# Optimization experiments

Hardware: AMD Instinct MI355X
Metric: run time of the kernel (lower is better)

Reference implementation:

```python
import jax, jax.numpy as jnp
import numpy as np

B, L, D = 8, 2048, 64

def setup_inputs() -> dict:
    key = jax.random.key(0)
    k1, k2 = jax.random.split(key)
    query = jax.random.normal(k1, (B, L, D), dtype=jnp.float32)
    key_t = jax.random.normal(k2, (B, L, D), dtype=jnp.float32)
    return {"query": query, "key": key_t}

def reference(query, key):
    d = query.shape[-1]
    # scores: [B, Lq, Lk] = Q K^T / sqrt(d)
    scores = jnp.einsum('bqd,bkd->bqk', query, key) / jnp.sqrt(jnp.asarray(d, query.dtype))
    weights = jax.nn.softmax(scores, axis=-1)  # dropout p=0.0 -> identity
    # output uses `key` as values, matching the original module
    return jnp.einsum('bqk,bkd->bqd', weights, key)
```

## Files before the change

kernel.cpp:

```cpp
#include <hip/hip_runtime.h>
#include <hip/hip_bf16.h>


#define LL 2048
#define DD 64
#define BQ 128
#define BK 64
#define KPAD 72
#define NSEG 4
#define NQB (LL / BQ)

typedef __attribute__((ext_vector_type(8))) short bf16x8;
typedef __attribute__((ext_vector_type(4))) float f32x4;
typedef __attribute__((ext_vector_type(4))) unsigned short u16x4;

static __device__ __forceinline__ unsigned short f2bf(float f) {
  unsigned u = __builtin_bit_cast(unsigned, f);
  u += 0x7fffu + ((u >> 16) & 1u);
  return (unsigned short)(u >> 16);
}
static __device__ __forceinline__ float bf2f(unsigned short h) {
  unsigned u = (unsigned)h << 16;
  return __builtin_bit_cast(float, u);
}

__global__ __launch_bounds__(256, 3) void attn_kernel(
    const float* __restrict__ Q, const float* __restrict__ K,
    float* __restrict__ O, u16x4* __restrict__ Opart,
    float* __restrict__ Lp, int seglen, int nseg) {
  __shared__ __attribute__((aligned(16))) unsigned short sKt[2][BK][KPAD];
  __shared__ __attribute__((aligned(16))) unsigned short sKtT[2][DD * KPAD];
  __shared__ __attribute__((aligned(16))) unsigned short sP[4][16][KPAD];

  const int tid  = threadIdx.x;
  const int wave = tid >> 6;
  const int lane = tid & 63;
  const int quad = lane >> 4;
  const int l16  = lane & 15;

  const int batch = blockIdx.y;
  const int seg   = blockIdx.z;
  const int q0w   = blockIdx.x * BQ + wave * 32;
  const int ngroups = gridDim.y * NQB;
  const int gq    = batch * NQB + blockIdx.x;

  const float qs = 0.125f * 1.44269504f;
  bf16x8 bq[2][2];
#pragma unroll
  for (int qt = 0; qt < 2; ++qt) {
    const float* qrow = Q + (size_t)(batch * LL + q0w + qt * 16 + l16) * DD;
#pragma unroll
    for (int ks = 0; ks < 2; ++ks) {
      const float* p = qrow + ks * 32 + quad * 8;
      float4 f0 = *(const float4*)(p);
      float4 f1 = *(const float4*)(p + 4);
      bf16x8 a;
      a[0] = (short)f2bf(f0.x * qs); a[1] = (short)f2bf(f0.y * qs);
      a[2] = (short)f2bf(f0.z * qs); a[3] = (short)f2bf(f0.w * qs);
      a[4] = (short)f2bf(f1.x * qs); a[5] = (short)f2bf(f1.y * qs);
      a[6] = (short)f2bf(f1.z * qs); a[7] = (short)f2bf(f1.w * qs);
      bq[qt][ks] = a;
    }
  }

  f32x4 oacc[2][4];
  float l_part[2];
#pragma unroll
  for (int qt = 0; qt < 2; ++qt) {
#pragma unroll
    for (int n = 0; n < 4; ++n) oacc[qt][n] = (f32x4){0.f, 0.f, 0.f, 0.f};
    l_part[qt] = 0.f;
  }

  const int niter = seglen / BK;
  const float* kbase = K + (size_t)(batch * LL + seg * seglen) * DD;
  const int kv_o  = tid >> 3;
  const int oc_o  = tid & 7;
  const int kv_o2 = kv_o + 32;

  float4 pf[2][2];
#pragma unroll
  for (int i = 0; i < 2; ++i) {
    int p = tid + i * 256;
    const float4* src = (const float4*)(kbase + (size_t)(p >> 3) * DD + (p & 7) * 8);
    pf[i][0] = src[0];
    pf[i][1] = src[1];
  }
#pragma unroll
  for (int i = 0; i < 2; ++i) {
    int kv = i ? kv_o2 : kv_o, oc = oc_o;
    unsigned short h[8];
    h[0] = f2bf(pf[i][0].x); h[1] = f2bf(pf[i][0].y);
    h[2] = f2bf(pf[i][0].z); h[3] = f2bf(pf[i][0].w);
    h[4] = f2bf(pf[i][1].x); h[5] = f2bf(pf[i][1].y);
    h[6] = f2bf(pf[i][1].z); h[7] = f2bf(pf[i][1].w);
    *(bf16x8*)&sKt[0][kv][oc * 8] = *(const bf16x8*)h;
    int swz = ((kv >> 3) ^ oc) & 7;
    unsigned short* dst = &sKtT[0][(oc * 8) * KPAD + swz * 8 + (kv & 7)];
#pragma unroll
    for (int j = 0; j < 8; ++j) dst[j * KPAD] = h[j];
  }
  __syncthreads();

  for (int t = 0; t < niter; ++t) {
    const int cur = t & 1;
    const int nxt = cur ^ 1;

    if (t + 1 < niter) {
      const float* kt = kbase + (size_t)(t + 1) * BK * DD;
#pragma unroll
      for (int i = 0; i < 2; ++i) {
        int p = tid + i * 256;
        const float4* src = (const float4*)(kt + (size_t)(p >> 3) * DD + (p & 7) * 8);
        pf[i][0] = src[0];
        pf[i][1] = src[1];
      }
    }

    bf16x8 pa[2][2];
#pragma unroll
    for (int qt = 0; qt < 2; ++qt) {
      f32x4 s[4];
#pragma unroll
      for (int mt = 0; mt < 4; ++mt) {
        bf16x8 k0 = *(const bf16x8*)&sKt[cur][mt * 16 + l16][quad * 8];
        bf16x8 k1 = *(const bf16x8*)&sKt[cur][mt * 16 + l16][32 + quad * 8];
        f32x4 z = (f32x4){0.f, 0.f, 0.f, 0.f};
        s[mt] = __builtin_amdgcn_mfma_f32_16x16x32_bf16(k0, bq[qt][0], z, 0, 0, 0);
        s[mt] = __builtin_amdgcn_mfma_f32_16x16x32_bf16(k1, bq[qt][1], s[mt], 0, 0, 0);
      }
#pragma unroll
      for (int mt = 0; mt < 4; ++mt) {
        u16x4 h;
#pragma unroll
        for (int r = 0; r < 4; ++r) {
          float p = __builtin_amdgcn_exp2f(s[mt][r]);
          l_part[qt] += p;
          h[r] = f2bf(p);
        }
        *(u16x4*)&sP[wave][l16][mt * 16 + quad * 4] = h;
      }
      pa[qt][0] = *(const bf16x8*)&sP[wave][l16][quad * 8];
      pa[qt][1] = *(const bf16x8*)&sP[wave][l16][32 + quad * 8];
    }

    if (t + 1 < niter) {
#pragma unroll
      for (int i = 0; i < 2; ++i) {
        int kv = i ? kv_o2 : kv_o, oc = oc_o;
        unsigned short h[8];
        h[0] = f2bf(pf[i][0].x); h[1] = f2bf(pf[i][0].y);
        h[2] = f2bf(pf[i][0].z); h[3] = f2bf(pf[i][0].w);
        h[4] = f2bf(pf[i][1].x); h[5] = f2bf(pf[i][1].y);
        h[6] = f2bf(pf[i][1].z); h[7] = f2bf(pf[i][1].w);
        *(bf16x8*)&sKt[nxt][kv][oc * 8] = *(const bf16x8*)h;
        int swz = ((kv >> 3) ^ oc) & 7;
        unsigned short* dst = &sKtT[nxt][(oc * 8) * KPAD + swz * 8 + (kv & 7)];
#pragma unroll
        for (int j = 0; j < 8; ++j) dst[j * KPAD] = h[j];
      }
    }

#pragma unroll
    for (int ks = 0; ks < 2; ++ks)
#pragma unroll
      for (int nt = 0; nt < 4; ++nt) {
        int d = nt * 16 + l16;
        bf16x8 b = *(const bf16x8*)
            &sKtT[cur][d * KPAD + (((ks * 4 + quad) ^ (d >> 3)) & 7) * 8];
        oacc[0][nt] = __builtin_amdgcn_mfma_f32_16x16x32_bf16(pa[0][ks], b, oacc[0][nt], 0, 0, 0);
        oacc[1][nt] = __builtin_amdgcn_mfma_f32_16x16x32_bf16(pa[1][ks], b, oacc[1][nt], 0, 0, 0);
      }

    __syncthreads();
  }

#pragma unroll
  for (int qt = 0; qt < 2; ++qt) {
    l_part[qt] += __shfl_xor(l_part[qt], 16);
    l_part[qt] += __shfl_xor(l_part[qt], 32);
  }

  if (nseg == 1) {
#pragma unroll
    for (int qt = 0; qt < 2; ++qt)
#pragma unroll
      for (int r = 0; r < 4; ++r) {
        float lr = __shfl(l_part[qt], (lane & 48) | (quad * 4 + r), 64);
        float invl = 1.0f / lr;
        float* orow = O + (size_t)(batch * LL + q0w + qt * 16 + quad * 4 + r) * DD;
#pragma unroll
        for (int nt = 0; nt < 4; ++nt)
          orow[nt * 16 + l16] = oacc[qt][nt][r] * invl;
      }
    return;
  }

  const size_t slotbase = ((size_t)seg * ngroups + gq) * 32 + wave * 8;
#pragma unroll
  for (int qt = 0; qt < 2; ++qt) {
#pragma unroll
    for (int nt = 0; nt < 4; ++nt) {
      u16x4 h;
      h[0] = f2bf(oacc[qt][nt][0]); h[1] = f2bf(oacc[qt][nt][1]);
      h[2] = f2bf(oacc[qt][nt][2]); h[3] = f2bf(oacc[qt][nt][3]);
      Opart[(slotbase + qt * 4 + nt) * 64 + lane] = h;
    }
    if (quad == 0)
      Lp[(((size_t)seg * ngroups + gq) * 8 + wave * 2 + qt) * 16 + l16] = l_part[qt];
  }
}

__global__ __launch_bounds__(256) void combine_kernel(
    const u16x4* __restrict__ Opart, const float* __restrict__ Lp,
    float* __restrict__ O, int nseg, int ngroups) {
  const int tid  = threadIdx.x;
  const int g    = blockIdx.x;
  const int slot = blockIdx.y * 4 + (tid >> 6);
  const int lane = tid & 63;
  const int quad = lane >> 4;
  const int l16  = lane & 15;
  const int wv = slot >> 3, qt = (slot >> 2) & 1, nt = slot & 3;

  f32x4 acc = (f32x4){0.f, 0.f, 0.f, 0.f};
  float den = 0.f;
  for (int s = 0; s < nseg; ++s) {
    u16x4 h = Opart[((size_t)(s * ngroups + g) * 32 + slot) * 64 + lane];
    acc[0] += bf2f(h[0]); acc[1] += bf2f(h[1]);
    acc[2] += bf2f(h[2]); acc[3] += bf2f(h[3]);
    den += Lp[((size_t)(s * ngroups + g) * 8 + wv * 2 + qt) * 16 + l16];
  }
  const int batch = g / NQB, qbx = g % NQB;
  const int rowbase = batch * LL + qbx * BQ + wv * 32 + qt * 16;
#pragma unroll
  for (int r = 0; r < 4; ++r) {
    float dr = __shfl(den, (lane & 48) | (quad * 4 + r), 64);
    O[(size_t)(rowbase + quad * 4 + r) * DD + nt * 16 + l16] = acc[r] / dr;
  }
}

extern "C" void kernel_launch(void* const* d_in, const int* in_sizes, int n_in,
                              void* d_out, int out_size, void* d_ws, size_t ws_size,
                              hipStream_t stream) {
  const float* Q = (const float*)d_in[0];
  const float* K = (const float*)d_in[1];
  float* O = (float*)d_out;
  int B = in_sizes[0] / (LL * DD);
  int ngroups = B * NQB;

  size_t opart_bytes = (size_t)NSEG * ngroups * 32 * 64 * sizeof(u16x4);
  size_t lp_bytes    = (size_t)NSEG * ngroups * 8 * 16 * sizeof(float);
  if (ws_size >= opart_bytes + lp_bytes) {
    u16x4* Opart = (u16x4*)d_ws;
    float* Lpp = (float*)((char*)d_ws + opart_bytes);
    dim3 grid(NQB, B, NSEG);
    attn_kernel<<<grid, 256, 0, stream>>>(Q, K, O, Opart, Lpp, LL / NSEG, NSEG);
    combine_kernel<<<dim3(ngroups, 8), 256, 0, stream>>>(Opart, Lpp, O, NSEG, ngroups);
  } else {
    dim3 grid(NQB, B, 1);
    attn_kernel<<<grid, 256, 0, stream>>>(Q, K, O, nullptr, nullptr, LL, 1);
  }
}
```

Baseline: 81.36 us.

## Switch attention to 32x32x16 MFMA with in-register P via permlane swap

Replaces the 16x16x32 MFMA tiles with 32x32x16 MFMA so each wave handles 32 query rows as one tile. The softmax probabilities are packed with v_cvt_pk_bf16_f32 and rearranged into the A-operand layout with v_permlane32_swap, which removes the shared-memory round trip through sP. Float-to-bf16 conversions also use the packed hardware convert, and the partial-output and denominator layouts plus the combine kernel are updated to match. This relies on gfx950-specific instructions and needs more accumulator registers per wave, which may affect occupancy.

```diff
diff --git a/kernel.cpp b/kernel.cpp
--- a/kernel.cpp
+++ b/kernel.cpp
@@ -1,5 +1,4 @@
 #include <hip/hip_runtime.h>
-#include <hip/hip_bf16.h>
 
 
 #define LL 2048
@@ -12,7 +11,10 @@
 
 typedef __attribute__((ext_vector_type(8))) short bf16x8;
 typedef __attribute__((ext_vector_type(4))) float f32x4;
+typedef __attribute__((ext_vector_type(16))) float f32x16;
 typedef __attribute__((ext_vector_type(4))) unsigned short u16x4;
+typedef __attribute__((ext_vector_type(2))) unsigned int u32x2;
+typedef __attribute__((ext_vector_type(4))) unsigned int u32x4;
 
 static __device__ __forceinline__ unsigned short f2bf(float f) {
   unsigned u = __builtin_bit_cast(unsigned, f);
@@ -22,6 +24,20 @@
 static __device__ __forceinline__ float bf2f(unsigned short h) {
   unsigned u = (unsigned)h << 16;
   return __builtin_bit_cast(float, u);
+}
+static __device__ __forceinline__ unsigned cvtpk(float lo, float hi) {
+  unsigned d;
+  asm("v_cvt_pk_bf16_f32 %0, %1, %2" : "=v"(d) : "v"(lo), "v"(hi));
+  return d;
+}
+#define PLSWAP(a, b) \
+  asm volatile("v_permlane32_swap_b32 %0, %1" : "+v"(a), "+v"(b))
+
+static __device__ __forceinline__ f32x16 zero16() {
+  f32x16 z;
+#pragma unroll
+  for (int i = 0; i < 16; ++i) z[i] = 0.f;
+  return z;
 }
 
 __global__ __launch_bounds__(256, 3) void attn_kernel(
@@ -30,13 +46,12 @@
     float* __restrict__ Lp, int seglen, int nseg) {
   __shared__ __attribute__((aligned(16))) unsigned short sKt[2][BK][KPAD];
   __shared__ __attribute__((aligned(16))) unsigned short sKtT[2][DD * KPAD];
-  __shared__ __attribute__((aligned(16))) unsigned short sP[4][16][KPAD];
 
   const int tid  = threadIdx.x;
   const int wave = tid >> 6;
   const int lane = tid & 63;
-  const int quad = lane >> 4;
-  const int l16  = lane & 15;
+  const int l31  = lane & 31;
+  const int hi   = lane >> 5;
 
   const int batch = blockIdx.y;
   const int seg   = blockIdx.z;
@@ -45,32 +60,27 @@
   const int gq    = batch * NQB + blockIdx.x;
 
   const float qs = 0.125f * 1.44269504f;
-  bf16x8 bq[2][2];
-#pragma unroll
-  for (int qt = 0; qt < 2; ++qt) {
-    const float* qrow = Q + (size_t)(batch * LL + q0w + qt * 16 + l16) * DD;
-#pragma unroll
-    for (int ks = 0; ks < 2; ++ks) {
-      const float* p = qrow + ks * 32 + quad * 8;
+  bf16x8 bq[4];
+  {
+    const float* qrow = Q + (size_t)(batch * LL + q0w + l31) * DD;
+#pragma unroll
+    for (int dc = 0; dc < 4; ++dc) {
+      const float* p = qrow + dc * 16 + hi * 8;
       float4 f0 = *(const float4*)(p);
       float4 f1 = *(const float4*)(p + 4);
-      bf16x8 a;
-      a[0] = (short)f2bf(f0.x * qs); a[1] = (short)f2bf(f0.y * qs);
-      a[2] = (short)f2bf(f0.z * qs); a[3] = (short)f2bf(f0.w * qs);
-      a[4] = (short)f2bf(f1.x * qs); a[5] = (short)f2bf(f1.y * qs);
-      a[6] = (short)f2bf(f1.z * qs); a[7] = (short)f2bf(f1.w * qs);
-      bq[qt][ks] = a;
-    }
-  }
-
-  f32x4 oacc[2][4];
-  float l_part[2];
-#pragma unroll
-  for (int qt = 0; qt < 2; ++qt) {
-#pragma unroll
-    for (int n = 0; n < 4; ++n) oacc[qt][n] = (f32x4){0.f, 0.f, 0.f, 0.f};
-    l_part[qt] = 0.f;
-  }
+      u32x4 d;
+      d[0] = cvtpk(f0.x * qs, f0.y * qs);
+      d[1] = cvtpk(f0.z * qs, f0.w * qs);
+      d[2] = cvtpk(f1.x * qs, f1.y * qs);
+      d[3] = cvtpk(f1.z * qs, f1.w * qs);
+      bq[dc] = __builtin_bit_cast(bf16x8, d);
+    }
+  }
+
+  f32x16 oacc[2];
+  oacc[0] = zero16();
+  oacc[1] = zero16();
+  float l_part = 0.f;
 
   const int niter = seglen / BK;
   const float* kbase = K + (size_t)(batch * LL + seg * seglen) * DD;
@@ -89,16 +99,19 @@
 #pragma unroll
   for (int i = 0; i < 2; ++i) {
     int kv = i ? kv_o2 : kv_o, oc = oc_o;
-    unsigned short h[8];
-    h[0] = f2bf(pf[i][0].x); h[1] = f2bf(pf[i][0].y);
-    h[2] = f2bf(pf[i][0].z); h[3] = f2bf(pf[i][0].w);
-    h[4] = f2bf(pf[i][1].x); h[5] = f2bf(pf[i][1].y);
-    h[6] = f2bf(pf[i][1].z); h[7] = f2bf(pf[i][1].w);
-    *(bf16x8*)&sKt[0][kv][oc * 8] = *(const bf16x8*)h;
+    u32x4 dw;
+    dw[0] = cvtpk(pf[i][0].x, pf[i][0].y);
+    dw[1] = cvtpk(pf[i][0].z, pf[i][0].w);
+    dw[2] = cvtpk(pf[i][1].x, pf[i][1].y);
+    dw[3] = cvtpk(pf[i][1].z, pf[i][1].w);
+    *(u32x4*)&sKt[0][kv][oc * 8] = dw;
     int swz = ((kv >> 3) ^ oc) & 7;
     unsigned short* dst = &sKtT[0][(oc * 8) * KPAD + swz * 8 + (kv & 7)];
 #pragma unroll
-    for (int j = 0; j < 8; ++j) dst[j * KPAD] = h[j];
+    for (int u = 0; u < 4; ++u) {
+      dst[(2 * u) * KPAD]     = (unsigned short)dw[u];
+      dst[(2 * u + 1) * KPAD] = (unsigned short)(dw[u] >> 16);
+    }
   }
   __syncthreads();
 
@@ -117,98 +130,100 @@
       }
     }
 
+    f32x16 s0 = zero16(), s1 = zero16();
+#pragma unroll
+    for (int dc = 0; dc < 4; ++dc) {
+      bf16x8 a0 = *(const bf16x8*)&sKt[cur][l31][dc * 16 + hi * 8];
+      bf16x8 a1 = *(const bf16x8*)&sKt[cur][32 + l31][dc * 16 + hi * 8];
+      s0 = __builtin_amdgcn_mfma_f32_32x32x16_bf16(a0, bq[dc], s0, 0, 0, 0);
+      s1 = __builtin_amdgcn_mfma_f32_32x32x16_bf16(a1, bq[dc], s1, 0, 0, 0);
+    }
+
     bf16x8 pa[2][2];
 #pragma unroll
-    for (int qt = 0; qt < 2; ++qt) {
-      f32x4 s[4];
-#pragma unroll
-      for (int mt = 0; mt < 4; ++mt) {
-        bf16x8 k0 = *(const bf16x8*)&sKt[cur][mt * 16 + l16][quad * 8];
-        bf16x8 k1 = *(const bf16x8*)&sKt[cur][mt * 16 + l16][32 + quad * 8];
-        f32x4 z = (f32x4){0.f, 0.f, 0.f, 0.f};
-        s[mt] = __builtin_amdgcn_mfma_f32_16x16x32_bf16(k0, bq[qt][0], z, 0, 0, 0);
-        s[mt] = __builtin_amdgcn_mfma_f32_16x16x32_bf16(k1, bq[qt][1], s[mt], 0, 0, 0);
-      }
-#pragma unroll
-      for (int mt = 0; mt < 4; ++mt) {
-        u16x4 h;
-#pragma unroll
-        for (int r = 0; r < 4; ++r) {
-          float p = __builtin_amdgcn_exp2f(s[mt][r]);
-          l_part[qt] += p;
-          h[r] = f2bf(p);
-        }
-        *(u16x4*)&sP[wave][l16][mt * 16 + quad * 4] = h;
-      }
-      pa[qt][0] = *(const bf16x8*)&sP[wave][l16][quad * 8];
-      pa[qt][1] = *(const bf16x8*)&sP[wave][l16][32 + quad * 8];
+    for (int tt = 0; tt < 2; ++tt) {
+      const f32x16 sv = tt ? s1 : s0;
+      unsigned w[8];
+#pragma unroll
+      for (int m = 0; m < 8; ++m) {
+        float pA = __builtin_amdgcn_exp2f(sv[2 * m]);
+        float pB = __builtin_amdgcn_exp2f(sv[2 * m + 1]);
+        l_part += pA + pB;
+        w[m] = cvtpk(pA, pB);
+      }
+      PLSWAP(w[0], w[2]);
+      PLSWAP(w[1], w[3]);
+      PLSWAP(w[4], w[6]);
+      PLSWAP(w[5], w[7]);
+      u32x4 lo = {w[0], w[1], w[2], w[3]};
+      u32x4 hh = {w[4], w[5], w[6], w[7]};
+      pa[tt][0] = __builtin_bit_cast(bf16x8, lo);
+      pa[tt][1] = __builtin_bit_cast(bf16x8, hh);
     }
 
     if (t + 1 < niter) {
 #pragma unroll
       for (int i = 0; i < 2; ++i) {
         int kv = i ? kv_o2 : kv_o, oc = oc_o;
-        unsigned short h[8];
-        h[0] = f2bf(pf[i][0].x); h[1] = f2bf(pf[i][0].y);
-        h[2] = f2bf(pf[i][0].z); h[3] = f2bf(pf[i][0].w);
-        h[4] = f2bf(pf[i][1].x); h[5] = f2bf(pf[i][1].y);
-        h[6] = f2bf(pf[i][1].z); h[7] = f2bf(pf[i][1].w);
-        *(bf16x8*)&sKt[nxt][kv][oc * 8] = *(const bf16x8*)h;
+        u32x4 dw;
+        dw[0] = cvtpk(pf[i][0].x, pf[i][0].y);
+        dw[1] = cvtpk(pf[i][0].z, pf[i][0].w);
+        dw[2] = cvtpk(pf[i][1].x, pf[i][1].y);
+        dw[3] = cvtpk(pf[i][1].z, pf[i][1].w);
+        *(u32x4*)&sKt[nxt][kv][oc * 8] = dw;
         int swz = ((kv >> 3) ^ oc) & 7;
         unsigned short* dst = &sKtT[nxt][(oc * 8) * KPAD + swz * 8 + (kv & 7)];
 #pragma unroll
-        for (int j = 0; j < 8; ++j) dst[j * KPAD] = h[j];
-      }
-    }
-
-#pragma unroll
-    for (int ks = 0; ks < 2; ++ks)
-#pragma unroll
-      for (int nt = 0; nt < 4; ++nt) {
-        int d = nt * 16 + l16;
+        for (int u = 0; u < 4; ++u) {
+          dst[(2 * u) * KPAD]     = (unsigned short)dw[u];
+          dst[(2 * u + 1) * KPAD] = (unsigned short)(dw[u] >> 16);
+        }
+      }
+    }
+
+#pragma unroll
+    for (int kk = 0; kk < 4; ++kk)
+#pragma unroll
+      for (int dt = 0; dt < 2; ++dt) {
+        const int d = dt * 32 + l31;
         bf16x8 b = *(const bf16x8*)
-            &sKtT[cur][d * KPAD + (((ks * 4 + quad) ^ (d >> 3)) & 7) * 8];
-        oacc[0][nt] = __builtin_amdgcn_mfma_f32_16x16x32_bf16(pa[0][ks], b, oacc[0][nt], 0, 0, 0);
-        oacc[1][nt] = __builtin_amdgcn_mfma_f32_16x16x32_bf16(pa[1][ks], b, oacc[1][nt], 0, 0, 0);
+            &sKtT[cur][d * KPAD + (((2 * kk + hi) ^ (d >> 3)) & 7) * 8];
+        oacc[dt] = __builtin_amdgcn_mfma_f32_32x32x16_bf16(
+            pa[kk >> 1][kk & 1], b, oacc[dt], 0, 0, 0);
       }
 
     __syncthreads();
   }
 
-#pragma unroll
-  for (int qt = 0; qt < 2; ++qt) {
-    l_part[qt] += __shfl_xor(l_part[qt], 16);
-    l_part[qt] += __shfl_xor(l_part[qt], 32);
-  }
+  float lt = l_part + __shfl_xor(l_part, 32);
 
   if (nseg == 1) {
 #pragma unroll
-    for (int qt = 0; qt < 2; ++qt)
-#pragma unroll
-      for (int r = 0; r < 4; ++r) {
-        float lr = __shfl(l_part[qt], (lane & 48) | (quad * 4 + r), 64);
-        float invl = 1.0f / lr;
-        float* orow = O + (size_t)(batch * LL + q0w + qt * 16 + quad * 4 + r) * DD;
-#pragma unroll
-        for (int nt = 0; nt < 4; ++nt)
-          orow[nt * 16 + l16] = oacc[qt][nt][r] * invl;
-      }
+    for (int dt = 0; dt < 2; ++dt)
+#pragma unroll
+      for (int g = 0; g < 4; ++g)
+#pragma unroll
+        for (int c = 0; c < 4; ++c) {
+          const int q = 8 * g + 4 * hi + c;
+          float lr = __shfl(lt, q, 64);
+          O[(size_t)(batch * LL + q0w + q) * DD + dt * 32 + l31] =
+              oacc[dt][4 * g + c] / lr;
+        }
     return;
   }
 
   const size_t slotbase = ((size_t)seg * ngroups + gq) * 32 + wave * 8;
 #pragma unroll
-  for (int qt = 0; qt < 2; ++qt) {
-#pragma unroll
-    for (int nt = 0; nt < 4; ++nt) {
-      u16x4 h;
-      h[0] = f2bf(oacc[qt][nt][0]); h[1] = f2bf(oacc[qt][nt][1]);
-      h[2] = f2bf(oacc[qt][nt][2]); h[3] = f2bf(oacc[qt][nt][3]);
-      Opart[(slotbase + qt * 4 + nt) * 64 + lane] = h;
-    }
-    if (quad == 0)
-      Lp[(((size_t)seg * ngroups + gq) * 8 + wave * 2 + qt) * 16 + l16] = l_part[qt];
-  }
+  for (int dt = 0; dt < 2; ++dt)
+#pragma unroll
+    for (int g = 0; g < 4; ++g) {
+      u32x2 dw;
+      dw[0] = cvtpk(oacc[dt][4 * g], oacc[dt][4 * g + 1]);
+      dw[1] = cvtpk(oacc[dt][4 * g + 2], oacc[dt][4 * g + 3]);
+      Opart[(slotbase + dt * 4 + g) * 64 + lane] = __builtin_bit_cast(u16x4, dw);
+    }
+  if (lane < 32)
+    Lp[(((size_t)seg * ngroups + gq) * 4 + wave) * 32 + lane] = lt;
 }
 
 __global__ __launch_bounds__(256) void combine_kernel(
@@ -218,25 +233,25 @@
   const int g    = blockIdx.x;
   const int slot = blockIdx.y * 4 + (tid >> 6);
   const int lane = tid & 63;
-  const int quad = lane >> 4;
-  const int l16  = lane & 15;
-  const int wv = slot >> 3, qt = (slot >> 2) & 1, nt = slot & 3;
+  const int l31  = lane & 31;
+  const int hi   = lane >> 5;
+  const int wv = slot >> 3, dt = (slot >> 2) & 1, rg = slot & 3;
 
   f32x4 acc = (f32x4){0.f, 0.f, 0.f, 0.f};
-  float den = 0.f;
+  f32x4 den = (f32x4){0.f, 0.f, 0.f, 0.f};
   for (int s = 0; s < nseg; ++s) {
     u16x4 h = Opart[((size_t)(s * ngroups + g) * 32 + slot) * 64 + lane];
     acc[0] += bf2f(h[0]); acc[1] += bf2f(h[1]);
     acc[2] += bf2f(h[2]); acc[3] += bf2f(h[3]);
-    den += Lp[((size_t)(s * ngroups + g) * 8 + wv * 2 + qt) * 16 + l16];
+    float4 d4 = *(const float4*)
+        &Lp[(((size_t)s * ngroups + g) * 4 + wv) * 32 + 8 * rg + 4 * hi];
+    den[0] += d4.x; den[1] += d4.y; den[2] += d4.z; den[3] += d4.w;
   }
   const int batch = g / NQB, qbx = g % NQB;
-  const int rowbase = batch * LL + qbx * BQ + wv * 32 + qt * 16;
-#pragma unroll
-  for (int r = 0; r < 4; ++r) {
-    float dr = __shfl(den, (lane & 48) | (quad * 4 + r), 64);
-    O[(size_t)(rowbase + quad * 4 + r) * DD + nt * 16 + l16] = acc[r] / dr;
-  }
+  const int rowbase = batch * LL + qbx * BQ + wv * 32 + 8 * rg + 4 * hi;
+#pragma unroll
+  for (int c = 0; c < 4; ++c)
+    O[(size_t)(rowbase + c) * DD + dt * 32 + l31] = acc[c] / den[c];
 }
 
 extern "C" void kernel_launch(void* const* d_in, const int* in_sizes, int n_in,
@@ -249,7 +264,7 @@
   int ngroups = B * NQB;
 
   size_t opart_bytes = (size_t)NSEG * ngroups * 32 * 64 * sizeof(u16x4);
-  size_t lp_bytes    = (size_t)NSEG * ngroups * 8 * 16 * sizeof(float);
+  size_t lp_bytes    = (size_t)NSEG * ngroups * 4 * 32 * sizeof(float);
   if (ws_size >= opart_bytes + lp_bytes) {
     u16x4* Opart = (u16x4*)d_ws;
     float* Lpp = (float*)((char*)d_ws + opart_bytes);
```

Result: faster. 77.40 us (-4.9%).
